# Optimization experiments

Hardware: AMD Instinct MI355X
Metric: run time of the kernel (lower is better)

Reference implementation:

```python
import jax, jax.numpy as jnp
import numpy as np

N_HEADS = 32
N_KV_HEADS = 8
HEAD_DIM = 64
ROPE_BASE = 10000.0


def setup_inputs() -> dict:
    key = jax.random.key(0)
    ks = jax.random.split(key, 5)
    B, T, C = 4, 1024, 2048
    kv_dim = N_KV_HEADS * HEAD_DIM
    scale = 0.02
    return {
        "x": jax.random.normal(ks[0], (B, T, C), dtype=jnp.float32),
        "Wq": jax.random.normal(ks[1], (C, C), dtype=jnp.float32) * scale,
        "Wk": jax.random.normal(ks[2], (C, kv_dim), dtype=jnp.float32) * scale,
        "Wv": jax.random.normal(ks[3], (C, kv_dim), dtype=jnp.float32) * scale,
        "Wp": jax.random.normal(ks[4], (C, C), dtype=jnp.float32) * scale,
    }


def _rotate_half(x):
    # interleaved rotation: (x0,x1,x2,x3,...) -> (-x1,x0,-x3,x2,...)
    x1 = x[..., ::2]
    x2 = x[..., 1::2]
    return jnp.stack((-x2, x1), axis=-1).reshape(x.shape)


def _rope_tables(T, dtype):
    inv_freq = 1.0 / (ROPE_BASE ** (jnp.arange(0, HEAD_DIM, 2, dtype=jnp.float32) / HEAD_DIM))
    freqs = jnp.arange(T, dtype=jnp.float32)[:, None] * inv_freq[None, :]  # (T, D/2)
    cos = jnp.repeat(jnp.cos(freqs), 2, axis=-1).astype(dtype)  # (T, D)
    sin = jnp.repeat(jnp.sin(freqs), 2, axis=-1).astype(dtype)
    return cos[None, None], sin[None, None]  # (1,1,T,D)


def reference(x, Wq, Wk, Wv, Wp):
    B, T, C = x.shape
    H, KV, D = N_HEADS, N_KV_HEADS, HEAD_DIM
    q = (x @ Wq).reshape(B, T, H, D).transpose(0, 2, 1, 3)   # (B,H,T,D)
    k = (x @ Wk).reshape(B, T, KV, D).transpose(0, 2, 1, 3)  # (B,KV,T,D)
    v = (x @ Wv).reshape(B, T, KV, D).transpose(0, 2, 1, 3)

    cos, sin = _rope_tables(T, x.dtype)
    q = q * cos + _rotate_half(q) * sin
    k = k * cos + _rotate_half(k) * sin

    rf = H // KV
    k = jnp.repeat(k, rf, axis=1)  # (B,H,T,D) GQA broadcast
    v = jnp.repeat(v, rf, axis=1)

    scores = jnp.einsum('bhqd,bhkd->bhqk', q, k) / jnp.sqrt(jnp.asarray(D, x.dtype))
    causal = jnp.tril(jnp.ones((T, T), dtype=bool))
    scores = jnp.where(causal[None, None], scores, -jnp.inf)
    attn = jax.nn.softmax(scores, axis=-1)
    out = jnp.einsum('bhqk,bhkd->bhqd', attn, v)  # (B,H,T,D)
    out = out.transpose(0, 2, 1, 3).reshape(B, T, C)
    return out @ Wp
```

## Files before the change

### kernel.cpp

```cpp
#include <hip/hip_runtime.h>
#include <hip/hip_bf16.h>


typedef __attribute__((ext_vector_type(4))) float f32x4;
typedef __attribute__((ext_vector_type(8))) short short8;

#define AS1C(p) ((const __attribute__((address_space(1))) void*)(p))
#define AS3(p)  ((__attribute__((address_space(3))) void*)(p))

__device__ __forceinline__ unsigned short f2bf(float f) {
  union { float f; unsigned int u; } x; x.f = f;
  unsigned int r = x.u + 0x7FFFu + ((x.u >> 16) & 1u);
  return (unsigned short)(r >> 16);
}

__device__ __forceinline__ unsigned short bfc(float f) {
  return __bfloat16_as_ushort(__float2bfloat16(f));
}

__device__ __forceinline__ float bf2f(unsigned short u) {
  union { float f; unsigned int v; } x; x.v = ((unsigned int)u) << 16;
  return x.f;
}

__device__ __forceinline__ float ex2(float x) {
  return __builtin_amdgcn_exp2f(x);
}

__global__ void rope_tab_kernel(float2* __restrict__ tab) {
  const int idx = blockIdx.x * 256 + threadIdx.x;
  const int t = idx >> 5, i = idx & 31;
  const float invf = exp2f(-(float)i * 0.41524101186092029f);
  float sv, cv;
  __sincosf((float)t * invf, &sv, &cv);
  tab[idx] = make_float2(cv, sv);
}

__global__ void cvt_bf16_kernel(const float* __restrict__ src,
                                unsigned short* __restrict__ dst, int n4) {
  int i = blockIdx.x * blockDim.x + threadIdx.x;
  if (i >= n4) return;
  const f32x4 v = *(const f32x4*)(src + (size_t)i * 4);
  ushort4 u = make_ushort4(f2bf(v[0]), f2bf(v[1]), f2bf(v[2]), f2bf(v[3]));
  *(ushort4*)(dst + (size_t)i * 4) = u;
}

__global__ void transpose_w_kernel(const float* __restrict__ Wq,
                                   const float* __restrict__ Wk,
                                   const float* __restrict__ Wv,
                                   const float* __restrict__ Wp,
                                   unsigned short* __restrict__ Wt,
                                   unsigned short* __restrict__ Wpt) {
  __shared__ float tile[32][33];
  const int z = blockIdx.z;
  const float* src;
  unsigned short* dst;
  int N, rowOff;
  float scale = 1.0f;
  if (z == 0)      { src = Wq; dst = Wt;  N = 2048; rowOff = 0;    scale = 0.18033688011112042f; }
  else if (z == 1) { src = Wk; dst = Wt;  N = 512;  rowOff = 2048; }
  else if (z == 2) { src = Wv; dst = Wt;  N = 512;  rowOff = 2560; }
  else             { src = Wp; dst = Wpt; N = 2048; rowOff = 0;    }
  const int n0 = blockIdx.x * 32, k0 = blockIdx.y * 32;
  if (n0 >= N) return;
  const int tx = threadIdx.x & 31, ty = threadIdx.x >> 5;
#pragma unroll
  for (int i = ty; i < 32; i += 8)
    tile[i][tx] = src[(size_t)(k0 + i) * N + (n0 + tx)];
  __syncthreads();
#pragma unroll
  for (int i = ty; i < 32; i += 8)
    dst[(size_t)(rowOff + n0 + i) * 2048 + (k0 + tx)] = f2bf(tile[tx][i] * scale);
}

__global__ void rope_bf16_kernel(const float2* __restrict__ tab,
                                 unsigned short* __restrict__ qb,
                                 unsigned short* __restrict__ kb) {
  const int idx = blockIdx.x * 256 + threadIdx.x;
  const int m = idx / 320;
  const int p = idx - m * 320;
  const int t = m & 1023;
  unsigned short* base;
  int col;
  if (p < 256) { base = qb + (size_t)m * 2048; col = p * 8; }
  else         { base = kb + (size_t)m * 512;  col = (p - 256) * 8; }
  const int i0 = (col & 63) >> 1;
  short8 v = *(short8*)(base + col);
  short8 o;
#pragma unroll
  for (int j = 0; j < 4; ++j) {
    const float2 cs = tab[t * 32 + i0 + j];
    const float x1 = bf2f((unsigned short)v[2 * j]);
    const float x2 = bf2f((unsigned short)v[2 * j + 1]);
    o[2 * j]     = (short)bfc(x1 * cs.x - x2 * cs.y);
    o[2 * j + 1] = (short)bfc(x2 * cs.x + x1 * cs.y);
  }
  *(short8*)(base + col) = o;
}

#define BAR() __builtin_amdgcn_s_barrier()

#define SA3(tile, half)                                                                  \
  do {                                                                                   \
    const unsigned short* p_ = Ap + (size_t)(m0 + (half) * 128 + sr) * 2048 + (tile) * 64 + sc; \
    const int d_ = (((tile) & 1) << 14) + ((half) << 13) + tid * 8;                      \
    __builtin_amdgcn_global_load_lds(AS1C(p_), AS3(&S[d_]), 16, 0, 0);                   \
    __builtin_amdgcn_global_load_lds(AS1C(p_ + (size_t)64 * 2048), AS3(&S[d_ + 4096]), 16, 0, 0); \
  } while (0)

#define SB3(tile, u)                                                                     \
  do {                                                                                   \
    const unsigned short* p_ = Bp + (size_t)(n0 + (u) * 64 + sr) * 2048 + (tile) * 64 + sc; \
    const int d_ = 32768 + ((tile) & 1) * 12288 + (u) * 4096 + tid * 8;                  \
    __builtin_amdgcn_global_load_lds(AS1C(p_), AS3(&S[d_]), 16, 0, 0);                   \
  } while (0)

#define RDA3(tile)                                                                       \
  _Pragma("unroll") for (int kk = 0; kk < 2; ++kk)                                       \
  _Pragma("unroll") for (int fm = 0; fm < 4; ++fm) {                                     \
    const int r_ = mg * 64 + fm * 16 + l15;                                              \
    af[kk][fm] = *(const short8*)&S[(((tile) & 1) << 14) + r_ * 64 +                     \
                                    (((kk << 2) | lg) ^ (r_ & 7)) * 8];                  \
  }

#define RDB3(tile, p)                                                                    \
  _Pragma("unroll") for (int kk = 0; kk < 2; ++kk)                                       \
  _Pragma("unroll") for (int jj = 0; jj < 2; ++jj) {                                     \
    const int r_ = ng * 96 + ((p) * 2 + jj) * 16 + l15;                                  \
    bf[kk][jj] = *(const short8*)&S[32768 + ((tile) & 1) * 12288 + r_ * 64 +             \
                                    (((kk << 2) | lg) ^ (r_ & 7)) * 8];                  \
  }

#define MM3(p)                                                                           \
  do {                                                                                   \
    __builtin_amdgcn_s_setprio(1);                                                       \
    _Pragma("unroll") for (int kk = 0; kk < 2; ++kk)                                     \
    _Pragma("unroll") for (int fm = 0; fm < 4; ++fm)                                     \
    _Pragma("unroll") for (int jj = 0; jj < 2; ++jj)                                     \
      acc[fm][(p) * 2 + jj] = __builtin_amdgcn_mfma_f32_16x16x32_bf16(                   \
          af[kk][fm], bf[kk][jj], acc[fm][(p) * 2 + jj], 0, 0, 0);                       \
    __builtin_amdgcn_s_setprio(0);                                                       \
  } while (0)

__global__ __launch_bounds__(512, 1) void gemm256x192_qkv_kernel(
    const unsigned short* __restrict__ Ap, const unsigned short* __restrict__ Bp,
    unsigned short* __restrict__ qb, unsigned short* __restrict__ kb,
    unsigned short* __restrict__ vt) {
  __shared__ unsigned short S[57344];
  const int tid = threadIdx.x;
  const int lane = tid & 63, w = tid >> 6;
  const int l15 = lane & 15, lg = lane >> 4;
  int lid = blockIdx.x + 16 * blockIdx.y;
  lid = (lid & 7) * 32 + (lid >> 3);
  const int m0 = (lid >> 4) * 256, n0 = (lid & 15) * 192;
  const int mg = w >> 1;
  const int ng = w & 1;
  const int sr = tid >> 3;
  const int sc = ((tid & 7) ^ (sr & 7)) << 3;
  const int NT = 32;

  f32x4 acc[4][6];
#pragma unroll
  for (int i = 0; i < 4; ++i)
#pragma unroll
    for (int j = 0; j < 6; ++j)
#pragma unroll
      for (int c = 0; c < 4; ++c) acc[i][j][c] = 0.f;

  SA3(0, 0); SA3(0, 1); SB3(0, 0); SB3(0, 1); SB3(0, 2);
  SA3(1, 0); SA3(1, 1); SB3(1, 0);
  asm volatile("s_waitcnt vmcnt(5)" ::: "memory");
  BAR();

  short8 af[2][4], bf[2][2];

  for (int t = 0; t < NT; t += 2) {
    const bool nl = (t + 2 < NT);
    RDA3(t); RDB3(t, 0);
    SB3(t + 1, 1); SB3(t + 1, 2);
    BAR();
    MM3(0);
    BAR();
    RDB3(t, 1);
    if (nl) SA3(t + 2, 0);
    BAR();
    MM3(1);
    BAR();
    RDB3(t, 2);
    if (nl) {
      SA3(t + 2, 1); SB3(t + 2, 0);
      asm volatile("s_waitcnt vmcnt(5)" ::: "memory");
    } else {
      asm volatile("s_waitcnt vmcnt(0)" ::: "memory");
    }
    BAR();
    MM3(2);
    BAR();
    RDA3(t + 1); RDB3(t + 1, 0);
    if (nl) { SB3(t + 2, 1); SB3(t + 2, 2); }
    BAR();
    MM3(0);
    BAR();
    RDB3(t + 1, 1);
    if (nl) SA3(t + 3, 0);
    BAR();
    MM3(1);
    BAR();
    RDB3(t + 1, 2);
    if (nl) {
      SA3(t + 3, 1); SB3(t + 3, 0);
      asm volatile("s_waitcnt vmcnt(5)" ::: "memory");
    }
    BAR();
    MM3(2);
    BAR();
  }

  const int colQK = n0 >= 2560 ? 0 : (n0 >= 2432 ? 2560 - n0 : 192);
#pragma unroll
  for (int fn = 0; fn < 6; ++fn) {
    const int col16 = n0 + ng * 96 + fn * 16;
    if (col16 < 2560) {
      const int colL = ng * 96 + fn * 16 + l15;
#pragma unroll
      for (int fm = 0; fm < 4; ++fm) {
        const int row = mg * 64 + fm * 16 + lg * 4;
#pragma unroll
        for (int r = 0; r < 4; ++r)
          S[(row + r) * 192 + colL] = bfc(acc[fm][fn][r]);
      }
    } else {
      const int dz = (col16 - 2560) >> 6;
      const int d = ((col16 - 2560) & 63) + l15;
#pragma unroll
      for (int fm = 0; fm < 4; ++fm) {
        const int row = m0 + mg * 64 + fm * 16 + lg * 4;
        const int z = (row >> 10) * 8 + dz;
        const int t0 = row & 1023;
        ushort4 u = make_ushort4(bfc(acc[fm][fn][0]), bfc(acc[fm][fn][1]),
                                 bfc(acc[fm][fn][2]), bfc(acc[fm][fn][3]));
        *(ushort4*)&vt[(size_t)z * 65536 + d * 1024 + t0] = u;
      }
    }
  }
  if (colQK > 0) {
    BAR();
    const int cpr = colQK >> 3;
    const int total = 256 * cpr;
    for (int c = tid; c < total; c += 512) {
      const int row = c / cpr;
      const int cc = (c - row * cpr) * 8;
      const short8 v = *(const short8*)&S[row * 192 + cc];
      const int gcol = n0 + cc;
      if (gcol < 2048)
        *(short8*)&qb[(size_t)(m0 + row) * 2048 + gcol] = v;
      else
        *(short8*)&kb[(size_t)(m0 + row) * 512 + (gcol - 2048)] = v;
    }
  }
}

#define SA2(tile, half)                                                                  \
  do {                                                                                   \
    const unsigned short* p_ = Ap + (size_t)(m0 + (half) * 128 + sr) * Kd + (tile) * 64 + sc; \
    const int d_ = (((tile) & 1) << 14) + ((half) << 13) + tid * 8;                      \
    __builtin_amdgcn_global_load_lds(AS1C(p_), AS3(&S[d_]), 16, 0, 0);                   \
    __builtin_amdgcn_global_load_lds(AS1C(p_ + (size_t)64 * Kd), AS3(&S[d_ + 4096]), 16, 0, 0); \
  } while (0)

#define SB2(tile)                                                                        \
  do {                                                                                   \
    const unsigned short* p_ = Bp + (size_t)(n0 + sr) * Kd + (tile) * 64 + sc;           \
    const int d_ = 32768 + (((tile) & 1) << 13) + tid * 8;                               \
    __builtin_amdgcn_global_load_lds(AS1C(p_), AS3(&S[d_]), 16, 0, 0);                   \
    __builtin_amdgcn_global_load_lds(AS1C(p_ + (size_t)64 * Kd), AS3(&S[d_ + 4096]), 16, 0, 0); \
  } while (0)

#define RDA2(tile, Msub)                                                                 \
  _Pragma("unroll") for (int kk = 0; kk < 2; ++kk)                                       \
  _Pragma("unroll") for (int fm = 0; fm < 4; ++fm) {                                     \
    const int r_ = (Msub) * 64 + fm * 16 + l15;                                          \
    af[kk][fm] = *(const short8*)&S[(((tile) & 1) << 14) + (ah << 13) + r_ * 64 +        \
                                    (((kk << 2) | lg) ^ (r_ & 7)) * 8];                  \
  }

#define RDB2(dst, tile)                                                                  \
  _Pragma("unroll") for (int kk = 0; kk < 2; ++kk)                                       \
  _Pragma("unroll") for (int j = 0; j < 2; ++j) {                                        \
    const int r_ = wn + j * 16 + l15;                                                    \
    dst[kk][j] = *(const short8*)&S[32768 + (((tile) & 1) << 13) + r_ * 64 +             \
                                    (((kk << 2) | lg) ^ (r_ & 7)) * 8];                  \
  }

#define MM2(Msub, bb)                                                                    \
  do {                                                                                   \
    __builtin_amdgcn_s_setprio(1);                                                       \
    _Pragma("unroll") for (int kk = 0; kk < 2; ++kk)                                     \
    _Pragma("unroll") for (int fm = 0; fm < 4; ++fm)                                     \
    _Pragma("unroll") for (int j = 0; j < 2; ++j)                                        \
      acc[(Msub) * 4 + fm][j] = __builtin_amdgcn_mfma_f32_16x16x32_bf16(                 \
          af[kk][fm], bb[kk][j], acc[(Msub) * 4 + fm][j], 0, 0, 0);                      \
    __builtin_amdgcn_s_setprio(0);                                                       \
  } while (0)

__global__ __launch_bounds__(512, 1) void gemm256x128_kernel(
    const unsigned short* __restrict__ Ap, const unsigned short* __restrict__ Bp,
    float* __restrict__ C, int K, int N) {
  __shared__ unsigned short S[49152];
  const int tid = threadIdx.x;
  const int lane = tid & 63, w = tid >> 6;
  const int l15 = lane & 15, lg = lane >> 4;
  const int nwgx = gridDim.x;
  const int nwg = nwgx * gridDim.y;
  int lid = blockIdx.x + nwgx * blockIdx.y;
  lid = (lid & 7) * (nwg >> 3) + (lid >> 3);
  const int m0 = (lid / nwgx) * 256, n0 = (lid % nwgx) * 128;
  const int ah = w >> 2;
  const int wn = (w & 3) * 32;
  const int NT = K >> 6;
  const int Kd = K;
  const int sr = tid >> 3;
  const int sc = ((tid & 7) ^ (sr & 7)) << 3;

  f32x4 acc[8][2];
#pragma unroll
  for (int i = 0; i < 8; ++i)
#pragma unroll
    for (int j = 0; j < 2; ++j)
#pragma unroll
      for (int c = 0; c < 4; ++c) acc[i][j][c] = 0.f;

  SB2(0); SA2(0, 0); SA2(0, 1); SB2(1); SA2(1, 0);
  asm volatile("s_waitcnt vmcnt(4)" ::: "memory");
  __builtin_amdgcn_s_barrier();

  short8 af[2][4], b0[2][2], b1[2][2];

  for (int t = 0; t < NT; t += 2) {
    const bool nl = (t + 2 < NT);
    RDA2(t, 0); RDB2(b0, t);
    SA2(t + 1, 1);
    BAR();
    MM2(0, b0);
    BAR();
    RDA2(t, 1);
    if (nl) {
      SB2(t + 2); SA2(t + 2, 0);
      asm volatile("s_waitcnt vmcnt(4)" ::: "memory");
    } else {
      asm volatile("s_waitcnt vmcnt(0)" ::: "memory");
    }
    BAR();
    MM2(1, b0);
    BAR();
    RDA2(t + 1, 0); RDB2(b1, t + 1);
    if (nl) SA2(t + 2, 1);
    BAR();
    MM2(0, b1);
    BAR();
    RDA2(t + 1, 1);
    if (nl) {
      SB2(t + 3); SA2(t + 3, 0);
      asm volatile("s_waitcnt vmcnt(4)" ::: "memory");
    }
    BAR();
    MM2(1, b1);
    BAR();
  }

#pragma unroll
  for (int fm8 = 0; fm8 < 8; ++fm8)
#pragma unroll
    for (int j = 0; j < 2; ++j) {
      const size_t base =
          (size_t)(m0 + ah * 128 + (fm8 >> 2) * 64 + (fm8 & 3) * 16 + lg * 4) * N +
          (n0 + wn + j * 16 + l15);
#pragma unroll
      for (int r = 0; r < 4; ++r) C[base + (size_t)r * N] = acc[fm8][j][r];
    }
}

__global__ __launch_bounds__(256) void attn_mfma_kernel(
    const unsigned short* __restrict__ qb, const unsigned short* __restrict__ kb,
    const unsigned short* __restrict__ vt, unsigned short* __restrict__ attnb) {
  int lid = blockIdx.x + 8 * (blockIdx.y + 32 * blockIdx.z);
  lid = (lid & 7) * 128 + (lid >> 3);
  const int bx = lid & 7, h = (lid >> 3) & 31, b = lid >> 8;
  const int kvh = h >> 2;
  __shared__ unsigned short S[20480];
  const int tid = threadIdx.x, lane = tid & 63, w = tid >> 6;
  const int l15 = lane & 15, lg = lane >> 4;
  const int rowbase = w * 16 + lg * 4;

  const int gi0 = w * 64 + lane;
  const int r0 = gi0 >> 3, g0 = (gi0 & 7) ^ (r0 & 7);
  const int gi1 = (4 + w) * 64 + lane;
  const int r1 = gi1 >> 3, g1 = (gi1 & 7) ^ (r1 & 7);

  const unsigned short* kbase = kb + (size_t)b * 1024 * 512 + kvh * 64;
  const unsigned short* vbase = vt + (size_t)(b * 8 + kvh) * 64 * 1024;

#define STAGE_KV(kOff, vOff, jj)                                                    \
  do {                                                                              \
    __builtin_amdgcn_global_load_lds(AS1C(kbase + ((jj) * 64 + r0) * 512 + g0 * 8), \
                                     AS3(&S[(kOff) + w * 512]), 16, 0, 0);          \
    __builtin_amdgcn_global_load_lds(AS1C(kbase + ((jj) * 64 + r1) * 512 + g1 * 8), \
                                     AS3(&S[(kOff) + (4 + w) * 512]), 16, 0, 0);    \
    __builtin_amdgcn_global_load_lds(AS1C(vbase + r0 * 1024 + (jj) * 64 + g0 * 8),  \
                                     AS3(&S[(vOff) + w * 512]), 16, 0, 0);          \
    __builtin_amdgcn_global_load_lds(AS1C(vbase + r1 * 1024 + (jj) * 64 + g1 * 8),  \
                                     AS3(&S[(vOff) + (4 + w) * 512]), 16, 0, 0);    \
  } while (0)

#define STAGE_Q(qt)                                                                     \
  do {                                                                                  \
    const size_t qr_ = (size_t)b * 1024 + (qt) * 64;                                    \
    __builtin_amdgcn_global_load_lds(AS1C(qb + (qr_ + r0) * 2048 + h * 64 + g0 * 8),    \
                                     AS3(&S[w * 512]), 16, 0, 0);                       \
    __builtin_amdgcn_global_load_lds(AS1C(qb + (qr_ + r1) * 2048 + h * 64 + g1 * 8),    \
                                     AS3(&S[(4 + w) * 512]), 16, 0, 0);                 \
  } while (0)

  const int qts0 = bx, qts1 = 15 - bx;

  short8 ones;
#pragma unroll
  for (int i = 0; i < 8; ++i) ones[i] = (short)0x3F80;

  STAGE_Q(qts0);
  STAGE_KV(4096, 12288, 0);
  __syncthreads();

  int g = 0;
  for (int sub = 0; sub < 2; ++sub) {
    const int qtc = sub ? qts1 : qts0;
    const size_t qrow0 = (size_t)b * 1024 + qtc * 64;

    short8 qf[2];
#pragma unroll
    for (int kk = 0; kk < 2; ++kk) {
      const int r = w * 16 + l15;
      const int gq = ((kk << 2) | lg) ^ (r & 7);
      qf[kk] = *(const short8*)&S[r * 64 + gq * 8];
    }

    f32x4 oa[4], oe;
#pragma unroll
    for (int r = 0; r < 4; ++r) oe[r] = 0.f;
#pragma unroll
    for (int fd = 0; fd < 4; ++fd)
#pragma unroll
      for (int r = 0; r < 4; ++r) oa[fd][r] = 0.f;

    for (int j = 0; j <= qtc; ++j, ++g) {
      const int cur = g & 1;
      const int kOff = 4096 + cur * 4096;
      const int vOff = 12288 + cur * 4096;
      if (g < 16) {
        const int nj = (g + 1 <= qts0) ? g + 1 : g - qts0;
        STAGE_KV(4096 + (cur ^ 1) * 4096, 12288 + (cur ^ 1) * 4096, nj);
      }

      f32x4 sa[4];
#pragma unroll
      for (int fn = 0; fn < 4; ++fn)
#pragma unroll
        for (int r = 0; r < 4; ++r) sa[fn][r] = 0.f;
#pragma unroll
      for (int kk = 0; kk < 2; ++kk) {
        short8 kf[4];
#pragma unroll
        for (int fn = 0; fn < 4; ++fn) {
          const int rkv = fn * 16 + l15;
          const int gk = ((kk << 2) | lg) ^ (rkv & 7);
          kf[fn] = *(const short8*)&S[kOff + rkv * 64 + gk * 8];
        }
        __builtin_amdgcn_s_setprio(1);
#pragma unroll
        for (int fn = 0; fn < 4; ++fn)
          sa[fn] = __builtin_amdgcn_mfma_f32_16x16x32_bf16(qf[kk], kf[fn], sa[fn], 0, 0, 0);
        __builtin_amdgcn_s_setprio(0);
      }

      if (j == qtc) {
#pragma unroll
        for (int r = 0; r < 4; ++r) {
          const int row = rowbase + r;
#pragma unroll
          for (int fn = 0; fn < 4; ++fn)
            if ((fn * 16 + l15) > row) sa[fn][r] = -INFINITY;
        }
      }
#pragma unroll
      for (int fn = 0; fn < 4; ++fn)
#pragma unroll
        for (int r = 0; r < 4; ++r) sa[fn][r] = ex2(sa[fn][r]);

#pragma unroll
      for (int r = 0; r < 4; ++r) {
        const int prow = rowbase + r;
#pragma unroll
        for (int fn = 0; fn < 4; ++fn) {
          const int col = fn * 16 + l15;
          const int gp = (col >> 3) ^ (prow & 7);
          S[prow * 64 + gp * 8 + (col & 7)] = bfc(sa[fn][r]);
        }
      }

#pragma unroll
      for (int kk = 0; kk < 2; ++kk) {
        const int rp = w * 16 + l15;
        const int gp = ((kk << 2) | lg) ^ (rp & 7);
        const short8 pf = *(const short8*)&S[rp * 64 + gp * 8];
        short8 vf[4];
#pragma unroll
        for (int fd = 0; fd < 4; ++fd) {
          const int rd = fd * 16 + l15;
          const int gv = ((kk << 2) | lg) ^ (rd & 7);
          vf[fd] = *(const short8*)&S[vOff + rd * 64 + gv * 8];
        }
        __builtin_amdgcn_s_setprio(1);
#pragma unroll
        for (int fd = 0; fd < 4; ++fd)
          oa[fd] = __builtin_amdgcn_mfma_f32_16x16x32_bf16(pf, vf[fd], oa[fd], 0, 0, 0);
        oe = __builtin_amdgcn_mfma_f32_16x16x32_bf16(pf, ones, oe, 0, 0, 0);
        __builtin_amdgcn_s_setprio(0);
      }

      __syncthreads();
    }

#pragma unroll
    for (int r = 0; r < 4; ++r) {
      const float inv = 1.0f / oe[r];
      const size_t row = qrow0 + rowbase + r;
#pragma unroll
      for (int fd = 0; fd < 4; ++fd)
        attnb[row * 2048 + h * 64 + fd * 16 + l15] = f2bf(oa[fd][r] * inv);
    }

    if (sub == 0) {
      STAGE_Q(qts1);
      __syncthreads();
    }
  }
#undef STAGE_KV
#undef STAGE_Q
}

extern "C" void kernel_launch(void* const* d_in, const int* in_sizes, int n_in,
                              void* d_out, int out_size, void* d_ws, size_t ws_size,
                              hipStream_t stream) {
  (void)in_sizes; (void)n_in; (void)out_size; (void)ws_size;
  const float* x  = (const float*)d_in[0];
  const float* Wq = (const float*)d_in[1];
  const float* Wk = (const float*)d_in[2];
  const float* Wv = (const float*)d_in[3];
  const float* Wp = (const float*)d_in[4];

  char* w = (char*)d_ws;
  unsigned short* xb    = (unsigned short*)(w);
  unsigned short* Wt    = (unsigned short*)(w + 16777216);
  unsigned short* Wpt   = (unsigned short*)(w + 29360128);
  unsigned short* qb    = (unsigned short*)(w + 37748736);
  unsigned short* kbuf  = (unsigned short*)(w + 54525952);
  unsigned short* vtb   = (unsigned short*)(w + 79691776);
  unsigned short* attnb = (unsigned short*)(w + 83886080);
  float2*         rtab  = (float2*)(w + 100663296);
  float* out = (float*)d_out;

  rope_tab_kernel<<<128, 256, 0, stream>>>(rtab);
  cvt_bf16_kernel<<<8192, 256, 0, stream>>>(x, xb, 2097152);
  transpose_w_kernel<<<dim3(64, 64, 4), 256, 0, stream>>>(Wq, Wk, Wv, Wp, Wt, Wpt);

  gemm256x192_qkv_kernel<<<dim3(16, 16), 512, 0, stream>>>(xb, Wt, qb, kbuf, vtb);
  rope_bf16_kernel<<<5120, 256, 0, stream>>>(rtab, qb, kbuf);
  attn_mfma_kernel<<<dim3(8, 32, 4), 256, 0, stream>>>(qb, kbuf, vtb, attnb);
  gemm256x128_kernel<<<dim3(16, 16), 512, 0, stream>>>(attnb, Wpt, out, 2048, 2048);
}
```

Baseline: 162.1 us.

## Process two 64-row query bands per attention block to reuse K/V tiles

```diff
diff --git a/kernel.cpp b/kernel.cpp
--- a/kernel.cpp
+++ b/kernel.cpp
@@ -383,19 +383,19 @@
 __global__ __launch_bounds__(256) void attn_mfma_kernel(
     const unsigned short* __restrict__ qb, const unsigned short* __restrict__ kb,
     const unsigned short* __restrict__ vt, unsigned short* __restrict__ attnb) {
-  int lid = blockIdx.x + 8 * (blockIdx.y + 32 * blockIdx.z);
-  lid = (lid & 7) * 128 + (lid >> 3);
-  const int bx = lid & 7, h = (lid >> 3) & 31, b = lid >> 8;
+  int lid = blockIdx.x + 4 * (blockIdx.y + 32 * blockIdx.z);
+  lid = (lid & 7) * 64 + (lid >> 3);
+  const int bx = lid & 3, h = (lid >> 2) & 31, b = lid >> 7;
   const int kvh = h >> 2;
-  __shared__ unsigned short S[20480];
+  __shared__ unsigned short S[24576];
   const int tid = threadIdx.x, lane = tid & 63, w = tid >> 6;
   const int l15 = lane & 15, lg = lane >> 4;
   const int rowbase = w * 16 + lg * 4;
 
-  const int gi0 = w * 64 + lane;
-  const int r0 = gi0 >> 3, g0 = (gi0 & 7) ^ (r0 & 7);
-  const int gi1 = (4 + w) * 64 + lane;
-  const int r1 = gi1 >> 3, g1 = (gi1 & 7) ^ (r1 & 7);
+  const int gi0 = w * 64 + lane;        const int r0 = gi0 >> 3, g0 = (gi0 & 7) ^ (r0 & 7);
+  const int gi1 = (4 + w) * 64 + lane;  const int r1 = gi1 >> 3, g1 = (gi1 & 7) ^ (r1 & 7);
+  const int gi2 = (8 + w) * 64 + lane;  const int r2 = gi2 >> 3, g2 = (gi2 & 7) ^ (r2 & 7);
+  const int gi3 = (12 + w) * 64 + lane; const int r3 = gi3 >> 3, g3 = (gi3 & 7) ^ (r3 & 7);
 
   const unsigned short* kbase = kb + (size_t)b * 1024 * 512 + kvh * 64;
   const unsigned short* vbase = vt + (size_t)(b * 8 + kvh) * 64 * 1024;
@@ -412,140 +412,161 @@
                                      AS3(&S[(vOff) + (4 + w) * 512]), 16, 0, 0);    \
   } while (0)
 
-#define STAGE_Q(qt)                                                                     \
+#define STAGE_Q128(qt)                                                                  \
   do {                                                                                  \
-    const size_t qr_ = (size_t)b * 1024 + (qt) * 64;                                    \
+    const size_t qr_ = (size_t)b * 1024 + (qt) * 128;                                   \
     __builtin_amdgcn_global_load_lds(AS1C(qb + (qr_ + r0) * 2048 + h * 64 + g0 * 8),    \
                                      AS3(&S[w * 512]), 16, 0, 0);                       \
     __builtin_amdgcn_global_load_lds(AS1C(qb + (qr_ + r1) * 2048 + h * 64 + g1 * 8),    \
                                      AS3(&S[(4 + w) * 512]), 16, 0, 0);                 \
-  } while (0)
-
-  const int qts0 = bx, qts1 = 15 - bx;
+    __builtin_amdgcn_global_load_lds(AS1C(qb + (qr_ + r2) * 2048 + h * 64 + g2 * 8),    \
+                                     AS3(&S[(8 + w) * 512]), 16, 0, 0);                 \
+    __builtin_amdgcn_global_load_lds(AS1C(qb + (qr_ + r3) * 2048 + h * 64 + g3 * 8),    \
+                                     AS3(&S[(12 + w) * 512]), 16, 0, 0);                \
+  } while (0)
+
+  const int qts0 = bx, qts1 = 7 - bx;
+  const int total0 = 2 * qts0 + 2;
 
   short8 ones;
 #pragma unroll
   for (int i = 0; i < 8; ++i) ones[i] = (short)0x3F80;
 
-  STAGE_Q(qts0);
-  STAGE_KV(4096, 12288, 0);
+  STAGE_Q128(qts0);
+  STAGE_KV(8192, 16384, 0);
   __syncthreads();
 
   int g = 0;
   for (int sub = 0; sub < 2; ++sub) {
-    const int qtc = sub ? qts1 : qts0;
-    const size_t qrow0 = (size_t)b * 1024 + qtc * 64;
-
-    short8 qf[2];
-#pragma unroll
-    for (int kk = 0; kk < 2; ++kk) {
-      const int r = w * 16 + l15;
-      const int gq = ((kk << 2) | lg) ^ (r & 7);
-      qf[kk] = *(const short8*)&S[r * 64 + gq * 8];
-    }
-
-    f32x4 oa[4], oe;
-#pragma unroll
-    for (int r = 0; r < 4; ++r) oe[r] = 0.f;
-#pragma unroll
-    for (int fd = 0; fd < 4; ++fd)
-#pragma unroll
-      for (int r = 0; r < 4; ++r) oa[fd][r] = 0.f;
-
-    for (int j = 0; j <= qtc; ++j, ++g) {
+    const int qt = sub ? qts1 : qts0;
+    const size_t qrow0 = (size_t)b * 1024 + qt * 128;
+
+    short8 qf[2][2];
+#pragma unroll
+    for (int band = 0; band < 2; ++band)
+#pragma unroll
+      for (int kk = 0; kk < 2; ++kk) {
+        const int r = band * 64 + w * 16 + l15;
+        const int gq = ((kk << 2) | lg) ^ (r & 7);
+        qf[band][kk] = *(const short8*)&S[r * 64 + gq * 8];
+      }
+
+    f32x4 oa[2][4], oe[2];
+#pragma unroll
+    for (int band = 0; band < 2; ++band) {
+#pragma unroll
+      for (int r = 0; r < 4; ++r) oe[band][r] = 0.f;
+#pragma unroll
+      for (int fd = 0; fd < 4; ++fd)
+#pragma unroll
+        for (int r = 0; r < 4; ++r) oa[band][fd][r] = 0.f;
+    }
+
+    const int jmax = 2 * qt + 1;
+    for (int j = 0; j <= jmax; ++j, ++g) {
       const int cur = g & 1;
-      const int kOff = 4096 + cur * 4096;
-      const int vOff = 12288 + cur * 4096;
-      if (g < 16) {
-        const int nj = (g + 1 <= qts0) ? g + 1 : g - qts0;
-        STAGE_KV(4096 + (cur ^ 1) * 4096, 12288 + (cur ^ 1) * 4096, nj);
+      const int kOff = 8192 + cur * 4096;
+      const int vOff = 16384 + cur * 4096;
+      if (g < 17) {
+        const int nj = (g + 1 < total0) ? (j + 1) : (g + 1 - total0);
+        STAGE_KV(8192 + (cur ^ 1) * 4096, 16384 + (cur ^ 1) * 4096, nj);
       }
 
-      f32x4 sa[4];
-#pragma unroll
-      for (int fn = 0; fn < 4; ++fn)
-#pragma unroll
-        for (int r = 0; r < 4; ++r) sa[fn][r] = 0.f;
-#pragma unroll
-      for (int kk = 0; kk < 2; ++kk) {
-        short8 kf[4];
-#pragma unroll
-        for (int fn = 0; fn < 4; ++fn) {
-          const int rkv = fn * 16 + l15;
-          const int gk = ((kk << 2) | lg) ^ (rkv & 7);
-          kf[fn] = *(const short8*)&S[kOff + rkv * 64 + gk * 8];
+#pragma unroll
+      for (int band = 0; band < 2; ++band) {
+        const int qtb = 2 * qt + band;
+        if (j > qtb) continue;
+
+        f32x4 sa[4];
+#pragma unroll
+        for (int fn = 0; fn < 4; ++fn)
+#pragma unroll
+          for (int r = 0; r < 4; ++r) sa[fn][r] = 0.f;
+#pragma unroll
+        for (int kk = 0; kk < 2; ++kk) {
+          short8 kf[4];
+#pragma unroll
+          for (int fn = 0; fn < 4; ++fn) {
+            const int rkv = fn * 16 + l15;
+            const int gk = ((kk << 2) | lg) ^ (rkv & 7);
+            kf[fn] = *(const short8*)&S[kOff + rkv * 64 + gk * 8];
+          }
+          __builtin_amdgcn_s_setprio(1);
+#pragma unroll
+          for (int fn = 0; fn < 4; ++fn)
+            sa[fn] = __builtin_amdgcn_mfma_f32_16x16x32_bf16(qf[band][kk], kf[fn],
+                                                             sa[fn], 0, 0, 0);
+          __builtin_amdgcn_s_setprio(0);
         }
-        __builtin_amdgcn_s_setprio(1);
+
+        if (j == qtb) {
+#pragma unroll
+          for (int r = 0; r < 4; ++r) {
+            const int row = rowbase + r;
+#pragma unroll
+            for (int fn = 0; fn < 4; ++fn)
+              if ((fn * 16 + l15) > row) sa[fn][r] = -INFINITY;
+          }
+        }
 #pragma unroll
         for (int fn = 0; fn < 4; ++fn)
-          sa[fn] = __builtin_amdgcn_mfma_f32_16x16x32_bf16(qf[kk], kf[fn], sa[fn], 0, 0, 0);
-        __builtin_amdgcn_s_setprio(0);
-      }
-
-      if (j == qtc) {
+#pragma unroll
+          for (int r = 0; r < 4; ++r) sa[fn][r] = ex2(sa[fn][r]);
+
 #pragma unroll
         for (int r = 0; r < 4; ++r) {
-          const int row = rowbase + r;
-#pragma unroll
-          for (int fn = 0; fn < 4; ++fn)
-            if ((fn * 16 + l15) > row) sa[fn][r] = -INFINITY;
+          const int prow = band * 64 + rowbase + r;
+#pragma unroll
+          for (int fn = 0; fn < 4; ++fn) {
+            const int col = fn * 16 + l15;
+            const int gp = (col >> 3) ^ (prow & 7);
+            S[prow * 64 + gp * 8 + (col & 7)] = bfc(sa[fn][r]);
+          }
+        }
+
+#pragma unroll
+        for (int kk = 0; kk < 2; ++kk) {
+          const int rp = band * 64 + w * 16 + l15;
+          const int gp = ((kk << 2) | lg) ^ (rp & 7);
+          const short8 pf = *(const short8*)&S[rp * 64 + gp * 8];
+          short8 vf[4];
+#pragma unroll
+          for (int fd = 0; fd < 4; ++fd) {
+            const int rd = fd * 16 + l15;
+            const int gv = ((kk << 2) | lg) ^ (rd & 7);
+            vf[fd] = *(const short8*)&S[vOff + rd * 64 + gv * 8];
+          }
+          __builtin_amdgcn_s_setprio(1);
+#pragma unroll
+          for (int fd = 0; fd < 4; ++fd)
+            oa[band][fd] = __builtin_amdgcn_mfma_f32_16x16x32_bf16(pf, vf[fd],
+                                                                   oa[band][fd], 0, 0, 0);
+          oe[band] = __builtin_amdgcn_mfma_f32_16x16x32_bf16(pf, ones, oe[band], 0, 0, 0);
+          __builtin_amdgcn_s_setprio(0);
         }
       }
-#pragma unroll
-      for (int fn = 0; fn < 4; ++fn)
-#pragma unroll
-        for (int r = 0; r < 4; ++r) sa[fn][r] = ex2(sa[fn][r]);
-
+
+      __syncthreads();
+    }
+
+#pragma unroll
+    for (int band = 0; band < 2; ++band)
 #pragma unroll
       for (int r = 0; r < 4; ++r) {
-        const int prow = rowbase + r;
-#pragma unroll
-        for (int fn = 0; fn < 4; ++fn) {
-          const int col = fn * 16 + l15;
-          const int gp = (col >> 3) ^ (prow & 7);
-          S[prow * 64 + gp * 8 + (col & 7)] = bfc(sa[fn][r]);
-        }
+        const float inv = 1.0f / oe[band][r];
+        const size_t row = qrow0 + band * 64 + rowbase + r;
+#pragma unroll
+        for (int fd = 0; fd < 4; ++fd)
+          attnb[row * 2048 + h * 64 + fd * 16 + l15] = f2bf(oa[band][fd][r] * inv);
       }
 
-#pragma unroll
-      for (int kk = 0; kk < 2; ++kk) {
-        const int rp = w * 16 + l15;
-        const int gp = ((kk << 2) | lg) ^ (rp & 7);
-        const short8 pf = *(const short8*)&S[rp * 64 + gp * 8];
-        short8 vf[4];
-#pragma unroll
-        for (int fd = 0; fd < 4; ++fd) {
-          const int rd = fd * 16 + l15;
-          const int gv = ((kk << 2) | lg) ^ (rd & 7);
-          vf[fd] = *(const short8*)&S[vOff + rd * 64 + gv * 8];
-        }
-        __builtin_amdgcn_s_setprio(1);
-#pragma unroll
-        for (int fd = 0; fd < 4; ++fd)
-          oa[fd] = __builtin_amdgcn_mfma_f32_16x16x32_bf16(pf, vf[fd], oa[fd], 0, 0, 0);
-        oe = __builtin_amdgcn_mfma_f32_16x16x32_bf16(pf, ones, oe, 0, 0, 0);
-        __builtin_amdgcn_s_setprio(0);
-      }
-
+    if (sub == 0) {
+      STAGE_Q128(qts1);
       __syncthreads();
     }
-
-#pragma unroll
-    for (int r = 0; r < 4; ++r) {
-      const float inv = 1.0f / oe[r];
-      const size_t row = qrow0 + rowbase + r;
-#pragma unroll
-      for (int fd = 0; fd < 4; ++fd)
-        attnb[row * 2048 + h * 64 + fd * 16 + l15] = f2bf(oa[fd][r] * inv);
-    }
-
-    if (sub == 0) {
-      STAGE_Q(qts1);
-      __syncthreads();
-    }
   }
 #undef STAGE_KV
-#undef STAGE_Q
+#undef STAGE_Q128
 }
 
 extern "C" void kernel_launch(void* const* d_in, const int* in_sizes, int n_in,
@@ -575,6 +596,6 @@
 
   gemm256x192_qkv_kernel<<<dim3(16, 16), 512, 0, stream>>>(xb, Wt, qb, kbuf, vtb);
   rope_bf16_kernel<<<5120, 256, 0, stream>>>(rtab, qb, kbuf);
-  attn_mfma_kernel<<<dim3(8, 32, 4), 256, 0, stream>>>(qb, kbuf, vtb, attnb);
+  attn_mfma_kernel<<<dim3(4, 32, 4), 256, 0, stream>>>(qb, kbuf, vtb, attnb);
   gemm256x128_kernel<<<dim3(16, 16), 512, 0, stream>>>(attnb, Wpt, out, 2048, 2048);
 }
```

Result: slower. 166.9 us (+3.0%).
